# Kernel optimization log

Hardware: AMD Instinct MI355X
Metric: run time of the kernel (lower is better)

Reference implementation:

```python
import jax, jax.numpy as jnp
import numpy as np

N_NODES = 100000


def _hetero_block(x, ei_t, ei_i, Wt, bt, Wi, bi, Wr, br):
    """ResidualGeneralHeteroConvBlock: per-edge-type linear message passing,
    'add' aggregation for temp_previous, 'mean' for intersects, summed across
    edge types, plus linear residual, ReLU."""
    n = x.shape[0]
    # transform-then-gather (cheaper than per-edge transform)
    ht = x @ Wt + bt                                   # [N, C]
    hi = x @ Wi + bi                                   # [N, C]
    # temp_previous: sum aggregation over incoming edges
    agg_t = jax.ops.segment_sum(ht[ei_t[0]], ei_t[1], num_segments=n)
    # intersects: mean aggregation
    sum_i = jax.ops.segment_sum(hi[ei_i[0]], ei_i[1], num_segments=n)
    cnt = jax.ops.segment_sum(jnp.ones((ei_i.shape[1],), x.dtype), ei_i[1],
                              num_segments=n)
    agg_i = sum_i / jnp.maximum(cnt, 1.0)[:, None]
    return jax.nn.relu(agg_t + agg_i + (x @ Wr + br))


def setup_inputs() -> dict:
    key = jax.random.key(0)
    ks = jax.random.split(key, 12)
    E = 2000000
    d = {
        "x": jax.random.normal(ks[0], (N_NODES, 6), jnp.float32),
        "edge_index_temp": jax.random.randint(ks[1], (2, E), 0, N_NODES),
        "edge_index_inter": jax.random.randint(ks[2], (2, E), 0, N_NODES),
        "W1t": jax.random.normal(ks[3], (6, 32), jnp.float32) * 0.3,
        "b1t": jnp.zeros((32,), jnp.float32),
        "W1i": jax.random.normal(ks[4], (6, 32), jnp.float32) * 0.3,
        "b1i": jnp.zeros((32,), jnp.float32),
        "W1r": jax.random.normal(ks[5], (6, 32), jnp.float32) * 0.3,
        "b1r": jnp.zeros((32,), jnp.float32),
        "W2t": jax.random.normal(ks[6], (32, 32), jnp.float32) * 0.15,
        "b2t": jnp.zeros((32,), jnp.float32),
        "W2i": jax.random.normal(ks[7], (32, 32), jnp.float32) * 0.15,
        "b2i": jnp.zeros((32,), jnp.float32),
        "W2r": jax.random.normal(ks[8], (32, 32), jnp.float32) * 0.15,
        "b2r": jnp.zeros((32,), jnp.float32),
        "Wc": jax.random.normal(ks[9], (32, 7), jnp.float32) * 0.15,
        "bc": jnp.zeros((7,), jnp.float32),
    }
    return d


def reference(x, edge_index_temp, edge_index_inter,
              W1t, b1t, W1i, b1i, W1r, b1r,
              W2t, b2t, W2i, b2i, W2r, b2r, Wc, bc):
    h = _hetero_block(x, edge_index_temp, edge_index_inter,
                      W1t, b1t, W1i, b1i, W1r, b1r)
    h = _hetero_block(h, edge_index_temp, edge_index_inter,
                      W2t, b2t, W2i, b2i, W2r, b2r)
    return h @ Wc + bc  # [N, num_classes]
```

## Files before the change

kernel.cpp:

```cpp
#include <hip/hip_runtime.h>


#define BLK 256
#define RN 512
#define KMAX 256
#define CAP 11264
#define CHUNK 4096

typedef unsigned short us8 __attribute__((ext_vector_type(8)));

__device__ inline unsigned short f2bf(float f) {
  unsigned u = __float_as_uint(f);
  return (unsigned short)((u + 0x7FFFu + ((u >> 16) & 1u)) >> 16);
}
__device__ inline float bf2f(unsigned short h) {
  return __uint_as_float(((unsigned)h) << 16);
}

__global__ __launch_bounds__(BLK) void k_prep(const float* __restrict__ x,
                                              unsigned short* __restrict__ xp,
                                              int* __restrict__ curT,
                                              int* __restrict__ curI, int N,
                                              int K) {
  int gid = blockIdx.x * BLK + threadIdx.x;
  if (gid < K) {
    curT[gid] = gid * CAP;
    curI[gid] = gid * CAP;
  }
  if (gid >= N * 8) return;
  int n = gid >> 3, c = gid & 7;
  xp[gid] = (c < 6) ? f2bf(x[n * 6 + c]) : (unsigned short)0;
}

__global__ __launch_bounds__(BLK) void k_bin3(
    const int* __restrict__ eiT, int ET, int* __restrict__ curT,
    int* __restrict__ binT, const int* __restrict__ eiI, int EI,
    int* __restrict__ curI, int* __restrict__ binI, int K) {
  const int* ei = blockIdx.y ? eiI : eiT;
  int E = blockIdx.y ? EI : ET;
  int* gcur = blockIdx.y ? curI : curT;
  int* binned = blockIdx.y ? binI : binT;
  int cs = blockIdx.x * CHUNK;
  if (cs >= E) return;
  int ce = min(E, cs + CHUNK);
  int cnt = ce - cs;
  __shared__ int ebuf[CHUNK];
  __shared__ unsigned char bbuf[CHUNK];
  __shared__ int hist[KMAX], cur[KMAX], gdelta[KMAX], s[KMAX];
  int t = threadIdx.x;
  hist[t] = 0;
  __syncthreads();
  for (int e = cs + t; e < ce; e += BLK) atomicAdd(&hist[ei[E + e] >> 9], 1);
  __syncthreads();
  int v = hist[t];
  s[t] = v;
  __syncthreads();
  for (int off = 1; off < KMAX; off <<= 1) {
    int x = (t >= off) ? s[t - off] : 0;
    __syncthreads();
    s[t] += x;
    __syncthreads();
  }
  int excl = s[t] - v;
  cur[t] = excl;
  if (t < K) gdelta[t] = atomicAdd(&gcur[t], v) - excl;
  __syncthreads();
  for (int e = cs + t; e < ce; e += BLK) {
    int src = ei[e];
    int d = ei[E + e];
    int b = d >> 9;
    int slot = atomicAdd(&cur[b], 1);
    ebuf[slot] = (src << 9) | (d & 511);
    bbuf[slot] = (unsigned char)b;
  }
  __syncthreads();
  for (int i = t; i < cnt; i += BLK) {
    int b = bbuf[i];
    __builtin_nontemporal_store(ebuf[i], &binned[i + gdelta[b]]);
  }
}

__global__ __launch_bounds__(512) void k_sortcsr2m(
    const int* __restrict__ binT, const int* __restrict__ curT,
    int* __restrict__ csrT, int* __restrict__ startT, int* __restrict__ degT,
    int* __restrict__ midT, const int* __restrict__ binI,
    const int* __restrict__ curI, int* __restrict__ csrI,
    int* __restrict__ startI, int* __restrict__ degI, int* __restrict__ midI,
    int N, int halfN) {
  const int* bin = blockIdx.y ? binI : binT;
  const int* cur = blockIdx.y ? curI : curT;
  int* csr = blockIdx.y ? csrI : csrT;
  int* start = blockIdx.y ? startI : startT;
  int* deg = blockIdx.y ? degI : degT;
  int* mid = blockIdx.y ? midI : midT;
  __shared__ int h[2 * RN], s[RN], c2[2 * RN];
  int t = threadIdx.x, b = blockIdx.x;
  int e0 = b * CAP;
  int cnt = min(cur[b] - e0, CAP);
  h[t] = 0;
  h[t + RN] = 0;
  __syncthreads();
  for (int i = t; i < cnt; i += 512) {
    int p = bin[e0 + i];
    int key = ((p & 511) << 1) | ((p >> 9) >= halfN ? 1 : 0);
    atomicAdd(&h[key], 1);
  }
  __syncthreads();
  int lo = h[2 * t], hi = h[2 * t + 1];
  int pair = lo + hi;
  s[t] = pair;
  __syncthreads();
  for (int off = 1; off < 512; off <<= 1) {
    int v = (t >= off) ? s[t - off] : 0;
    __syncthreads();
    s[t] += v;
    __syncthreads();
  }
  int excl = s[t] - pair;
  c2[2 * t] = excl;
  c2[2 * t + 1] = excl + lo;
  int n = b * RN + t;
  if (n < N) {
    start[n] = e0 + excl;
    deg[n] = pair;
    mid[n] = e0 + excl + lo;
  }
  __syncthreads();
  for (int i = t; i < cnt; i += 512) {
    int p = bin[e0 + i];
    int key = ((p & 511) << 1) | ((p >> 9) >= halfN ? 1 : 0);
    int pos = atomicAdd(&c2[key], 1);
    csr[e0 + pos] = p >> 9;
  }
}

#define GN1 64
__global__ __launch_bounds__(BLK) void k_g1c1(
    const unsigned short* __restrict__ xp, const float* __restrict__ x,
    const int* __restrict__ startT, const int* __restrict__ degT,
    const int* __restrict__ csrT, const int* __restrict__ startI,
    const int* __restrict__ degI, const int* __restrict__ csrI,
    const float* __restrict__ Wt, const float* __restrict__ bt,
    const float* __restrict__ Wi, const float* __restrict__ bi,
    const float* __restrict__ Wr, const float* __restrict__ br,
    unsigned short* __restrict__ h1b, int N) {
  __shared__ float sGT[GN1 * 8], sGI[GN1 * 8], sx[GN1 * 6];
  __shared__ float sWt[192], sWi[192], sWr[192], sb[96];
  __shared__ float sdT[GN1], sdI[GN1];
  int t = threadIdx.x, b = blockIdx.x;
  if (t < 192) { sWt[t] = Wt[t]; sWi[t] = Wi[t]; sWr[t] = Wr[t]; }
  if (t < 32) { sb[t] = bt[t]; sb[32 + t] = bi[t]; sb[64 + t] = br[t]; }
  for (int i = t; i < GN1 * 6; i += BLK) {
    int g = b * GN1 * 6 + i;
    sx[i] = (g < N * 6) ? x[g] : 0.0f;
  }
  int nl = t >> 2, et = (t >> 1) & 1, sub = t & 1;
  int n = b * GN1 + nl;
  float a0 = 0.f, a1 = 0.f, a2 = 0.f, a3 = 0.f;
  int d = 0;
  if (n < N) {
    const int* startA = et ? startI : startT;
    const int* degA = et ? degI : degT;
    const int* csrA = et ? csrI : csrT;
    int s0 = startA[n];
    d = degA[n];
    const int* c = csrA + s0;
    int i = 0;
    for (; i + 4 <= d; i += 4) {
      int r0 = c[i], r1 = c[i + 1], r2 = c[i + 2], r3 = c[i + 3];
      ushort4 v0 = *(const ushort4*)(xp + (size_t)r0 * 8 + sub * 4);
      ushort4 v1 = *(const ushort4*)(xp + (size_t)r1 * 8 + sub * 4);
      ushort4 v2 = *(const ushort4*)(xp + (size_t)r2 * 8 + sub * 4);
      ushort4 v3 = *(const ushort4*)(xp + (size_t)r3 * 8 + sub * 4);
      a0 += (bf2f(v0.x) + bf2f(v1.x)) + (bf2f(v2.x) + bf2f(v3.x));
      a1 += (bf2f(v0.y) + bf2f(v1.y)) + (bf2f(v2.y) + bf2f(v3.y));
      a2 += (bf2f(v0.z) + bf2f(v1.z)) + (bf2f(v2.z) + bf2f(v3.z));
      a3 += (bf2f(v0.w) + bf2f(v1.w)) + (bf2f(v2.w) + bf2f(v3.w));
    }
    for (; i < d; ++i) {
      int r0 = c[i];
      ushort4 v0 = *(const ushort4*)(xp + (size_t)r0 * 8 + sub * 4);
      a0 += bf2f(v0.x); a1 += bf2f(v0.y); a2 += bf2f(v0.z); a3 += bf2f(v0.w);
    }
  }
  float* dst = et ? sGI : sGT;
  int base = nl * 8 + sub * 4;
  dst[base + 0] = a0; dst[base + 1] = a1;
  dst[base + 2] = a2; dst[base + 3] = a3;
  if (sub == 0) {
    if (et) sdI[nl] = (float)d;
    else    sdT[nl] = (float)d;
  }
  __syncthreads();
  for (int idx = t; idx < GN1 * 32; idx += BLK) {
    int m = idx >> 5, j = idx & 31;
    int nn = b * GN1 + m;
    if (nn >= N) break;
    float fdT = sdT[m], fdI = sdI[m];
    float invI = 1.0f / fmaxf(fdI, 1.0f);
    float gate = (fdI > 0.0f) ? 1.0f : 0.0f;
    float acc = fdT * sb[j] + gate * sb[32 + j] + sb[64 + j];
#pragma unroll
    for (int k = 0; k < 6; ++k) {
      acc += sGT[m * 8 + k] * sWt[k * 32 + j];
      acc += sGI[m * 8 + k] * invI * sWi[k * 32 + j];
      acc += sx[m * 6 + k] * sWr[k * 32 + j];
    }
    h1b[(size_t)nn * 32 + j] = f2bf(fmaxf(acc, 0.0f));
  }
}

__device__ inline void accum8(const unsigned short* __restrict__ tab,
                              const int* __restrict__ csr, int i0, int i1,
                              int c8, float* a) {
  int i = i0;
  for (; i + 4 <= i1; i += 4) {
    int r0 = csr[i], r1 = csr[i + 1], r2 = csr[i + 2], r3 = csr[i + 3];
    us8 v0 = *(const us8*)(tab + (size_t)r0 * 32 + c8);
    us8 v1 = *(const us8*)(tab + (size_t)r1 * 32 + c8);
    us8 v2 = *(const us8*)(tab + (size_t)r2 * 32 + c8);
    us8 v3 = *(const us8*)(tab + (size_t)r3 * 32 + c8);
#pragma unroll
    for (int k = 0; k < 8; ++k)
      a[k] += (bf2f(v0[k]) + bf2f(v1[k])) + (bf2f(v2[k]) + bf2f(v3[k]));
  }
  for (; i < i1; ++i) {
    int r0 = csr[i];
    us8 v0 = *(const us8*)(tab + (size_t)r0 * 32 + c8);
#pragma unroll
    for (int k = 0; k < 8; ++k) a[k] += bf2f(v0[k]);
  }
}

__global__ __launch_bounds__(BLK) void k_gather2(
    const unsigned short* __restrict__ h1b, const int* __restrict__ startT,
    const int* __restrict__ degT, const int* __restrict__ midT,
    const int* __restrict__ csrT, const int* __restrict__ startI,
    const int* __restrict__ degI, const int* __restrict__ midI,
    const int* __restrict__ csrI, float* __restrict__ aggT,
    float* __restrict__ aggI, int N) {
  const int* start = blockIdx.y ? startI : startT;
  const int* deg = blockIdx.y ? degI : degT;
  const int* mid = blockIdx.y ? midI : midT;
  const int* csr = blockIdx.y ? csrI : csrT;
  float* agg = blockIdx.y ? aggI : aggT;
  int gid = blockIdx.x * BLK + threadIdx.x;
  int n = gid >> 2;
  if (n >= N) return;
  int c8 = (gid & 3) * 8;
  float a[8] = {0.f, 0.f, 0.f, 0.f, 0.f, 0.f, 0.f, 0.f};
  int s0 = start[n], d = deg[n], m = mid[n];
  accum8(h1b, csr, s0, m, c8, a);
  accum8(h1b, csr, m, s0 + d, c8, a);
  float* p = agg + (size_t)n * 32 + c8;
#pragma unroll
  for (int k = 0; k < 8; ++k) __builtin_nontemporal_store(a[k], p + k);
}

#define CN 64
__global__ __launch_bounds__(BLK) void k_combine2cls(
    const float* __restrict__ aggT, const float* __restrict__ aggI,
    const unsigned short* __restrict__ h1b, const int* __restrict__ degT,
    const int* __restrict__ degI, const float* __restrict__ Wt,
    const float* __restrict__ bt, const float* __restrict__ Wi,
    const float* __restrict__ bi, const float* __restrict__ Wr,
    const float* __restrict__ br, const float* __restrict__ Wc,
    const float* __restrict__ bc, float* __restrict__ out, int N) {
  __shared__ float hTs[CN * 32], hIs[CN * 32], hRs[CN * 32], hs2[CN * 32];
  __shared__ float sWc[224], sbc[7], sb[96];
  __shared__ float sdT[CN], sdI[CN];
  int t = threadIdx.x;
  int j = t & 31, ln = t >> 5;
  float wt[32], wi[32], wr[32];
#pragma unroll
  for (int k = 0; k < 32; ++k) {
    wt[k] = Wt[k * 32 + j];
    wi[k] = Wi[k * 32 + j];
    wr[k] = Wr[k * 32 + j];
  }
  int node0 = blockIdx.x * CN;
  size_t gbase = (size_t)node0 * 32;
  {
    const float4* sT = (const float4*)(aggT + gbase);
    const float4* sI = (const float4*)(aggI + gbase);
    ((float4*)hTs)[t] = sT[t];
    ((float4*)hTs)[t + 256] = sT[t + 256];
    ((float4*)hIs)[t] = sI[t];
    ((float4*)hIs)[t + 256] = sI[t + 256];
    us8 v = ((const us8*)(h1b + gbase))[t];
    float4 lo = {bf2f(v[0]), bf2f(v[1]), bf2f(v[2]), bf2f(v[3])};
    float4 hi = {bf2f(v[4]), bf2f(v[5]), bf2f(v[6]), bf2f(v[7])};
    ((float4*)hRs)[2 * t] = lo;
    ((float4*)hRs)[2 * t + 1] = hi;
  }
  if (t < 224) sWc[t] = Wc[t];
  if (t < 7) sbc[t] = bc[t];
  if (t < 32) { sb[t] = bt[t]; sb[32 + t] = bi[t]; sb[64 + t] = br[t]; }
  if (t < CN) {
    int n = node0 + t;
    sdT[t] = (n < N) ? (float)degT[n] : 0.f;
    sdI[t] = (n < N) ? (float)degI[n] : 0.f;
  }
  __syncthreads();
#pragma unroll
  for (int it = 0; it < CN / 8; ++it) {
    int li = it * 8 + ln;
    float dT = sdT[li], dI = sdI[li];
    float invI = 1.0f / fmaxf(dI, 1.0f);
    float gate = (dI > 0.0f) ? 1.0f : 0.0f;
    float aT = 0.f, aI = 0.f, aR = 0.f;
    const float4* hT4 = (const float4*)(hTs + li * 32);
    const float4* hI4 = (const float4*)(hIs + li * 32);
    const float4* hR4 = (const float4*)(hRs + li * 32);
#pragma unroll
    for (int kk = 0; kk < 8; ++kk) {
      float4 a = hT4[kk], bI = hI4[kk], r = hR4[kk];
      aT += a.x * wt[kk * 4 + 0] + a.y * wt[kk * 4 + 1] +
            a.z * wt[kk * 4 + 2] + a.w * wt[kk * 4 + 3];
      aI += bI.x * wi[kk * 4 + 0] + bI.y * wi[kk * 4 + 1] +
            bI.z * wi[kk * 4 + 2] + bI.w * wi[kk * 4 + 3];
      aR += r.x * wr[kk * 4 + 0] + r.y * wr[kk * 4 + 1] +
            r.z * wr[kk * 4 + 2] + r.w * wr[kk * 4 + 3];
    }
    float acc = dT * sb[j] + gate * sb[32 + j] + sb[64 + j] + aT + invI * aI + aR;
    hs2[li * 32 + j] = fmaxf(acc, 0.0f);
  }
  __syncthreads();
  if (t < 224) {
#pragma unroll
    for (int pass = 0; pass < CN * 7 / 224; ++pass) {
      int o = pass * 224 + t;
      int m = o / 7, jc = o - m * 7;
      int n = node0 + m;
      if (n < N) {
        float a = sbc[jc];
        const float* hp = hs2 + m * 32;
#pragma unroll
        for (int k = 0; k < 32; ++k) a += hp[k] * sWc[k * 7 + jc];
        out[(size_t)n * 7 + jc] = a;
      }
    }
  }
}

extern "C" void kernel_launch(void* const* d_in, const int* in_sizes, int n_in,
                              void* d_out, int out_size, void* d_ws,
                              size_t ws_size, hipStream_t stream) {
  const float* x   = (const float*)d_in[0];
  const int* ei_t  = (const int*)d_in[1];
  const int* ei_i  = (const int*)d_in[2];
  const float* W1t = (const float*)d_in[3];
  const float* b1t = (const float*)d_in[4];
  const float* W1i = (const float*)d_in[5];
  const float* b1i = (const float*)d_in[6];
  const float* W1r = (const float*)d_in[7];
  const float* b1r = (const float*)d_in[8];
  const float* W2t = (const float*)d_in[9];
  const float* b2t = (const float*)d_in[10];
  const float* W2i = (const float*)d_in[11];
  const float* b2i = (const float*)d_in[12];
  const float* W2r = (const float*)d_in[13];
  const float* b2r = (const float*)d_in[14];
  const float* Wc  = (const float*)d_in[15];
  const float* bc  = (const float*)d_in[16];
  float* out = (float*)d_out;

  const int N  = in_sizes[0] / 6;
  const int E  = in_sizes[1] / 2;
  const int Ei = in_sizes[2] / 2;
  const int K  = (N + RN - 1) / RN;
  const int halfN = N >> 1;

  float* aggT = (float*)d_ws;
  float* aggI = aggT + (size_t)N * 32;
  unsigned short* h1b = (unsigned short*)(aggI + (size_t)N * 32);
  unsigned short* xp  = h1b + (size_t)N * 32;
  int* curT   = (int*)(xp + (size_t)N * 8);
  int* curI   = curT + KMAX;
  int* startT = curI + KMAX;
  int* degT   = startT + N;
  int* midT   = degT + N;
  int* startI = midT + N;
  int* degI   = startI + N;
  int* midI   = degI + N;
  int* binT   = midI + N;
  int* binI   = binT + (size_t)K * CAP;
  int* csrT   = binI + (size_t)K * CAP;
  int* csrI   = csrT + (size_t)K * CAP;

  const int gN8  = (N * 8 + BLK - 1) / BLK;
  const int gG1  = (N + GN1 - 1) / GN1;
  const int gG2  = (N * 4 + BLK - 1) / BLK;
  const int gC2  = (N + CN - 1) / CN;
  const int Emax = (E > Ei) ? E : Ei;
  const int gBin = (Emax + CHUNK - 1) / CHUNK;

  k_prep<<<gN8, BLK, 0, stream>>>(x, xp, curT, curI, N, K);
  k_bin3<<<dim3(gBin, 2), BLK, 0, stream>>>(ei_t, E, curT, binT, ei_i, Ei,
                                            curI, binI, K);
  k_sortcsr2m<<<dim3(K, 2), 512, 0, stream>>>(binT, curT, csrT, startT, degT,
                                              midT, binI, curI, csrI, startI,
                                              degI, midI, N, halfN);

  k_g1c1<<<gG1, BLK, 0, stream>>>(xp, x, startT, degT, csrT, startI, degI,
                                  csrI, W1t, b1t, W1i, b1i, W1r, b1r, h1b, N);

  k_gather2<<<dim3(gG2, 2), BLK, 0, stream>>>(h1b, startT, degT, midT, csrT,
                                              startI, degI, midI, csrI, aggT,
                                              aggI, N);
  k_combine2cls<<<gC2, BLK, 0, stream>>>(aggT, aggI, h1b, degT, degI, W2t,
                                         b2t, W2i, b2i, W2r, b2r, Wc, bc, out,
                                         N);
}
```

Before: 264.3 us.

## Store CSR source indices as 16-bit offsets relative to half-table bases

CSR source indices are stored as unsigned short offsets, split by whether the source lies in the lower or upper half of the node range, with the half base added back at gather time. This halves CSR index traffic in both gather kernels. The first-layer gather also splits each node's edge list into two halves across extra threads (GN1 reduced to 32) so each half uses its own table base. It relies on halfN fitting in 16 bits (N=100000 gives halfN=50000) and adds a small shared-memory reduction of the two partial sums.

```diff
diff --git a/kernel.cpp b/kernel.cpp
--- a/kernel.cpp
+++ b/kernel.cpp
@@ -82,14 +82,14 @@
 
 __global__ __launch_bounds__(512) void k_sortcsr2m(
     const int* __restrict__ binT, const int* __restrict__ curT,
-    int* __restrict__ csrT, int* __restrict__ startT, int* __restrict__ degT,
-    int* __restrict__ midT, const int* __restrict__ binI,
-    const int* __restrict__ curI, int* __restrict__ csrI,
-    int* __restrict__ startI, int* __restrict__ degI, int* __restrict__ midI,
-    int N, int halfN) {
+    unsigned short* __restrict__ csrT, int* __restrict__ startT,
+    int* __restrict__ degT, int* __restrict__ midT,
+    const int* __restrict__ binI, const int* __restrict__ curI,
+    unsigned short* __restrict__ csrI, int* __restrict__ startI,
+    int* __restrict__ degI, int* __restrict__ midI, int N, int halfN) {
   const int* bin = blockIdx.y ? binI : binT;
   const int* cur = blockIdx.y ? curI : curT;
-  int* csr = blockIdx.y ? csrI : csrT;
+  unsigned short* csr = blockIdx.y ? csrI : csrT;
   int* start = blockIdx.y ? startI : startT;
   int* deg = blockIdx.y ? degI : degT;
   int* mid = blockIdx.y ? midI : midT;
@@ -128,66 +128,73 @@
   __syncthreads();
   for (int i = t; i < cnt; i += 512) {
     int p = bin[e0 + i];
-    int key = ((p & 511) << 1) | ((p >> 9) >= halfN ? 1 : 0);
+    int src = p >> 9;
+    int hiFlag = (src >= halfN) ? 1 : 0;
+    int key = ((p & 511) << 1) | hiFlag;
     int pos = atomicAdd(&c2[key], 1);
-    csr[e0 + pos] = p >> 9;
-  }
-}
-
-#define GN1 64
+    csr[e0 + pos] = (unsigned short)(src - hiFlag * halfN);
+  }
+}
+
+#define GN1 32
 __global__ __launch_bounds__(BLK) void k_g1c1(
     const unsigned short* __restrict__ xp, const float* __restrict__ x,
     const int* __restrict__ startT, const int* __restrict__ degT,
-    const int* __restrict__ csrT, const int* __restrict__ startI,
-    const int* __restrict__ degI, const int* __restrict__ csrI,
+    const int* __restrict__ midT, const unsigned short* __restrict__ csrT,
+    const int* __restrict__ startI, const int* __restrict__ degI,
+    const int* __restrict__ midI, const unsigned short* __restrict__ csrI,
     const float* __restrict__ Wt, const float* __restrict__ bt,
     const float* __restrict__ Wi, const float* __restrict__ bi,
     const float* __restrict__ Wr, const float* __restrict__ br,
-    unsigned short* __restrict__ h1b, int N) {
-  __shared__ float sGT[GN1 * 8], sGI[GN1 * 8], sx[GN1 * 6];
+    unsigned short* __restrict__ h1b, int N, int halfN) {
+  __shared__ float sGT[GN1 * 16], sGI[GN1 * 16], sx[GN1 * 6];
   __shared__ float sWt[192], sWi[192], sWr[192], sb[96];
   __shared__ float sdT[GN1], sdI[GN1];
   int t = threadIdx.x, b = blockIdx.x;
   if (t < 192) { sWt[t] = Wt[t]; sWi[t] = Wi[t]; sWr[t] = Wr[t]; }
   if (t < 32) { sb[t] = bt[t]; sb[32 + t] = bi[t]; sb[64 + t] = br[t]; }
-  for (int i = t; i < GN1 * 6; i += BLK) {
-    int g = b * GN1 * 6 + i;
-    sx[i] = (g < N * 6) ? x[g] : 0.0f;
-  }
-  int nl = t >> 2, et = (t >> 1) & 1, sub = t & 1;
+  if (t < GN1 * 6) {
+    int g = b * GN1 * 6 + t;
+    sx[t] = (g < N * 6) ? x[g] : 0.0f;
+  }
+  int nl = t >> 3, et = (t >> 2) & 1, half = (t >> 1) & 1, sub = t & 1;
   int n = b * GN1 + nl;
   float a0 = 0.f, a1 = 0.f, a2 = 0.f, a3 = 0.f;
   int d = 0;
   if (n < N) {
     const int* startA = et ? startI : startT;
     const int* degA = et ? degI : degT;
-    const int* csrA = et ? csrI : csrT;
+    const int* midA = et ? midI : midT;
+    const unsigned short* csrA = et ? csrI : csrT;
     int s0 = startA[n];
     d = degA[n];
-    const int* c = csrA + s0;
-    int i = 0;
-    for (; i + 4 <= d; i += 4) {
-      int r0 = c[i], r1 = c[i + 1], r2 = c[i + 2], r3 = c[i + 3];
-      ushort4 v0 = *(const ushort4*)(xp + (size_t)r0 * 8 + sub * 4);
-      ushort4 v1 = *(const ushort4*)(xp + (size_t)r1 * 8 + sub * 4);
-      ushort4 v2 = *(const ushort4*)(xp + (size_t)r2 * 8 + sub * 4);
-      ushort4 v3 = *(const ushort4*)(xp + (size_t)r3 * 8 + sub * 4);
+    int m = midA[n];
+    int i0 = half ? m : s0;
+    int i1 = half ? (s0 + d) : m;
+    const unsigned short* tab = xp + (half ? (size_t)halfN * 8 : 0) + sub * 4;
+    int i = i0;
+    for (; i + 4 <= i1; i += 4) {
+      int r0 = csrA[i], r1 = csrA[i + 1], r2 = csrA[i + 2], r3 = csrA[i + 3];
+      ushort4 v0 = *(const ushort4*)(tab + (size_t)r0 * 8);
+      ushort4 v1 = *(const ushort4*)(tab + (size_t)r1 * 8);
+      ushort4 v2 = *(const ushort4*)(tab + (size_t)r2 * 8);
+      ushort4 v3 = *(const ushort4*)(tab + (size_t)r3 * 8);
       a0 += (bf2f(v0.x) + bf2f(v1.x)) + (bf2f(v2.x) + bf2f(v3.x));
       a1 += (bf2f(v0.y) + bf2f(v1.y)) + (bf2f(v2.y) + bf2f(v3.y));
       a2 += (bf2f(v0.z) + bf2f(v1.z)) + (bf2f(v2.z) + bf2f(v3.z));
       a3 += (bf2f(v0.w) + bf2f(v1.w)) + (bf2f(v2.w) + bf2f(v3.w));
     }
-    for (; i < d; ++i) {
-      int r0 = c[i];
-      ushort4 v0 = *(const ushort4*)(xp + (size_t)r0 * 8 + sub * 4);
+    for (; i < i1; ++i) {
+      int r0 = csrA[i];
+      ushort4 v0 = *(const ushort4*)(tab + (size_t)r0 * 8);
       a0 += bf2f(v0.x); a1 += bf2f(v0.y); a2 += bf2f(v0.z); a3 += bf2f(v0.w);
     }
   }
   float* dst = et ? sGI : sGT;
-  int base = nl * 8 + sub * 4;
+  int base = nl * 16 + half * 8 + sub * 4;
   dst[base + 0] = a0; dst[base + 1] = a1;
   dst[base + 2] = a2; dst[base + 3] = a3;
-  if (sub == 0) {
+  if (half == 0 && sub == 0) {
     if (et) sdI[nl] = (float)d;
     else    sdT[nl] = (float)d;
   }
@@ -202,8 +209,10 @@
     float acc = fdT * sb[j] + gate * sb[32 + j] + sb[64 + j];
 #pragma unroll
     for (int k = 0; k < 6; ++k) {
-      acc += sGT[m * 8 + k] * sWt[k * 32 + j];
-      acc += sGI[m * 8 + k] * invI * sWi[k * 32 + j];
+      float gT = sGT[m * 16 + k] + sGT[m * 16 + 8 + k];
+      float gI = sGI[m * 16 + k] + sGI[m * 16 + 8 + k];
+      acc += gT * sWt[k * 32 + j];
+      acc += gI * invI * sWi[k * 32 + j];
       acc += sx[m * 6 + k] * sWr[k * 32 + j];
     }
     h1b[(size_t)nn * 32 + j] = f2bf(fmaxf(acc, 0.0f));
@@ -211,22 +220,22 @@
 }
 
 __device__ inline void accum8(const unsigned short* __restrict__ tab,
-                              const int* __restrict__ csr, int i0, int i1,
-                              int c8, float* a) {
+                              const unsigned short* __restrict__ csr, int i0,
+                              int i1, float* a) {
   int i = i0;
   for (; i + 4 <= i1; i += 4) {
     int r0 = csr[i], r1 = csr[i + 1], r2 = csr[i + 2], r3 = csr[i + 3];
-    us8 v0 = *(const us8*)(tab + (size_t)r0 * 32 + c8);
-    us8 v1 = *(const us8*)(tab + (size_t)r1 * 32 + c8);
-    us8 v2 = *(const us8*)(tab + (size_t)r2 * 32 + c8);
-    us8 v3 = *(const us8*)(tab + (size_t)r3 * 32 + c8);
+    us8 v0 = *(const us8*)(tab + (size_t)r0 * 32);
+    us8 v1 = *(const us8*)(tab + (size_t)r1 * 32);
+    us8 v2 = *(const us8*)(tab + (size_t)r2 * 32);
+    us8 v3 = *(const us8*)(tab + (size_t)r3 * 32);
 #pragma unroll
     for (int k = 0; k < 8; ++k)
       a[k] += (bf2f(v0[k]) + bf2f(v1[k])) + (bf2f(v2[k]) + bf2f(v3[k]));
   }
   for (; i < i1; ++i) {
     int r0 = csr[i];
-    us8 v0 = *(const us8*)(tab + (size_t)r0 * 32 + c8);
+    us8 v0 = *(const us8*)(tab + (size_t)r0 * 32);
 #pragma unroll
     for (int k = 0; k < 8; ++k) a[k] += bf2f(v0[k]);
   }
@@ -235,14 +244,14 @@
 __global__ __launch_bounds__(BLK) void k_gather2(
     const unsigned short* __restrict__ h1b, const int* __restrict__ startT,
     const int* __restrict__ degT, const int* __restrict__ midT,
-    const int* __restrict__ csrT, const int* __restrict__ startI,
+    const unsigned short* __restrict__ csrT, const int* __restrict__ startI,
     const int* __restrict__ degI, const int* __restrict__ midI,
-    const int* __restrict__ csrI, float* __restrict__ aggT,
-    float* __restrict__ aggI, int N) {
+    const unsigned short* __restrict__ csrI, float* __restrict__ aggT,
+    float* __restrict__ aggI, int N, int halfN) {
   const int* start = blockIdx.y ? startI : startT;
   const int* deg = blockIdx.y ? degI : degT;
   const int* mid = blockIdx.y ? midI : midT;
-  const int* csr = blockIdx.y ? csrI : csrT;
+  const unsigned short* csr = blockIdx.y ? csrI : csrT;
   float* agg = blockIdx.y ? aggI : aggT;
   int gid = blockIdx.x * BLK + threadIdx.x;
   int n = gid >> 2;
@@ -250,8 +259,8 @@
   int c8 = (gid & 3) * 8;
   float a[8] = {0.f, 0.f, 0.f, 0.f, 0.f, 0.f, 0.f, 0.f};
   int s0 = start[n], d = deg[n], m = mid[n];
-  accum8(h1b, csr, s0, m, c8, a);
-  accum8(h1b, csr, m, s0 + d, c8, a);
+  accum8(h1b + c8, csr, s0, m, a);
+  accum8(h1b + (size_t)halfN * 32 + c8, csr, m, s0 + d, a);
   float* p = agg + (size_t)n * 32 + c8;
 #pragma unroll
   for (int k = 0; k < 8; ++k) __builtin_nontemporal_store(a[k], p + k);
@@ -385,8 +394,8 @@
   int* midI   = degI + N;
   int* binT   = midI + N;
   int* binI   = binT + (size_t)K * CAP;
-  int* csrT   = binI + (size_t)K * CAP;
-  int* csrI   = csrT + (size_t)K * CAP;
+  unsigned short* csrT = (unsigned short*)(binI + (size_t)K * CAP);
+  unsigned short* csrI = csrT + (size_t)K * CAP;
 
   const int gN8  = (N * 8 + BLK - 1) / BLK;
   const int gG1  = (N + GN1 - 1) / GN1;
@@ -402,12 +411,13 @@
                                               midT, binI, curI, csrI, startI,
                                               degI, midI, N, halfN);
 
-  k_g1c1<<<gG1, BLK, 0, stream>>>(xp, x, startT, degT, csrT, startI, degI,
-                                  csrI, W1t, b1t, W1i, b1i, W1r, b1r, h1b, N);
+  k_g1c1<<<gG1, BLK, 0, stream>>>(xp, x, startT, degT, midT, csrT, startI,
+                                  degI, midI, csrI, W1t, b1t, W1i, b1i, W1r,
+                                  b1r, h1b, N, halfN);
 
   k_gather2<<<dim3(gG2, 2), BLK, 0, stream>>>(h1b, startT, degT, midT, csrT,
                                               startI, degI, midI, csrI, aggT,
-                                              aggI, N);
+                                              aggI, N, halfN);
   k_combine2cls<<<gC2, BLK, 0, stream>>>(aggT, aggI, h1b, degT, degI, W2t,
                                          b2t, W2i, b2i, W2r, b2r, Wc, bc, out,
                                          N);
```

Result: faster. 252.3 us (median of 3 runs) (-4.5%).
